# Optimization experiments

Hardware: AMD Instinct MI355X
Metric: run time of the kernel (lower is better)

Reference implementation:

```python
import jax, jax.numpy as jnp
import numpy as np

# ---- MACE hyperparameters (match init_kwargs) ----
R_MAX = 5.0      # radial cutoff
P_CUT = 6        # polynomial cutoff exponent
NUM_BESSEL = 8
C = 32           # hidden channels
N_NODES = 50000
N_EDGES = 800000
N_SPECIES = 10
N_GRAPHS = 32
AVG_NEIGH = 16.0
RADIAL_HIDDEN = 64
N_LM = 9                      # (lmax+1)^2, lmax=2
L_OF_LM = np.array([0, 1, 1, 1, 2, 2, 2, 2, 2])


def _sph_harm_l2(v):
    """Real spherical harmonics up to l=2, e3nn 'component' normalization.
    v: [E,3] unit vectors -> [E,9]."""
    x, y, z = v[:, 0], v[:, 1], v[:, 2]
    s3, s5, s15 = 3.0 ** 0.5, 5.0 ** 0.5, 15.0 ** 0.5
    return jnp.stack([
        jnp.ones_like(x),                 # l=0
        s3 * x, s3 * y, s3 * z,           # l=1
        s15 * x * y, s15 * y * z,         # l=2
        (s5 / 2.0) * (3.0 * z * z - 1.0),
        s15 * x * z,
        (s15 / 2.0) * (x * x - y * y),
    ], axis=-1)


def _radial_basis(r):
    """Bessel basis * polynomial cutoff. r: [E] -> [E, NUM_BESSEL]."""
    n = jnp.arange(1, NUM_BESSEL + 1, dtype=r.dtype)
    safe_r = jnp.maximum(r, 1e-9)
    bessel = jnp.sqrt(2.0 / R_MAX) * jnp.sin(n * jnp.pi * safe_r[:, None] / R_MAX) / safe_r[:, None]
    u = r / R_MAX
    p = float(P_CUT)
    fcut = (1.0 - ((p + 1.0) * (p + 2.0) / 2.0) * u ** P_CUT
            + p * (p + 2.0) * u ** (P_CUT + 1)
            - (p * (p + 1.0) / 2.0) * u ** (P_CUT + 2))
    fcut = jnp.where(u < 1.0, fcut, 0.0)
    return bessel * fcut[:, None]


def setup_inputs() -> dict:
    key = jax.random.key(0)
    ks = jax.random.split(key, 12)
    positions = 1.5 * jax.random.normal(ks[0], (N_NODES, 3), dtype=jnp.float32)
    shifts = jnp.zeros((N_EDGES, 3), dtype=jnp.float32)
    species = jax.random.randint(ks[1], (N_NODES,), 0, N_SPECIES)
    node_attrs = jax.nn.one_hot(species, N_SPECIES, dtype=jnp.float32)
    edge_index = jax.random.randint(ks[2], (2, N_EDGES), 0, N_NODES)
    batch = jnp.sort(jax.random.randint(ks[3], (N_NODES,), 0, N_GRAPHS))
    # learned parameters
    W_embed = jax.random.normal(ks[4], (N_SPECIES, C), jnp.float32) / np.sqrt(N_SPECIES)
    rW1 = jax.random.normal(ks[5], (NUM_BESSEL, RADIAL_HIDDEN), jnp.float32) / np.sqrt(NUM_BESSEL)
    rb1 = jnp.zeros((RADIAL_HIDDEN,), jnp.float32)
    rW2 = jax.random.normal(ks[6], (RADIAL_HIDDEN, RADIAL_HIDDEN), jnp.float32) / np.sqrt(RADIAL_HIDDEN)
    rb2 = jnp.zeros((RADIAL_HIDDEN,), jnp.float32)
    rW3 = jax.random.normal(ks[7], (RADIAL_HIDDEN, C * 3), jnp.float32) / np.sqrt(RADIAL_HIDDEN)
    W_mix = jax.random.normal(ks[8], (3, C, C), jnp.float32) / np.sqrt(C)   # per-l channel mixing
    w_quad = jax.random.normal(ks[9], (3,), jnp.float32) * 0.1              # correlation-2 invariant weights
    W_readout = jax.random.normal(ks[10], (C,), jnp.float32) / np.sqrt(C)
    atomic_energies = jax.random.normal(ks[11], (N_SPECIES,), jnp.float32)
    return {"node_attrs": node_attrs, "positions": positions, "shifts": shifts,
            "W_embed": W_embed, "rW1": rW1, "rb1": rb1, "rW2": rW2, "rb2": rb2,
            "rW3": rW3, "W_mix": W_mix, "w_quad": w_quad, "W_readout": W_readout,
            "atomic_energies": atomic_energies, "edge_index": edge_index, "batch": batch}


def reference(node_attrs, positions, shifts, W_embed, rW1, rb1, rW2, rb2, rW3,
              W_mix, w_quad, W_readout, atomic_energies, edge_index, batch):
    sender, receiver = edge_index[0], edge_index[1]
    # edge vectors / lengths (get_edge_vectors_and_lengths)
    vec = positions[receiver] - positions[sender] + shifts          # [E,3]
    length = jnp.linalg.norm(vec, axis=-1)                          # [E]
    unit = vec / jnp.maximum(length, 1e-9)[:, None]
    # radial embedding (Bessel * polynomial cutoff) -> MLP -> per-(channel,l) weights
    rb = _radial_basis(length)                                      # [E,8]
    h1 = jax.nn.silu(rb @ rW1 + rb1)
    h2 = jax.nn.silu(h1 @ rW2 + rb2)
    R = (h2 @ rW3).reshape(-1, C, 3)                                # [E,C,3]
    Y = _sph_harm_l2(unit)                                          # [E,9]
    # node embedding (LinearNodeEmbeddingBlock)
    h = node_attrs @ W_embed                                        # [N,C]
    # channelwise CG tensor product message (scalar source x Y_l -> l) + scatter-sum
    l_of_lm = jnp.asarray(L_OF_LM)
    msg = R[:, :, l_of_lm] * h[sender][:, :, None] * Y[:, None, :]  # [E,C,9]
    A = jax.ops.segment_sum(msg, receiver, num_segments=N_NODES) / AVG_NEIGH  # [N,C,9]
    # per-l linear channel mixing (o3.Linear)
    W_lm = W_mix[l_of_lm]                                           # [9,C,C]
    A2 = jnp.einsum('mcd,ncm->ndm', W_lm, A)                        # [N,C,9]
    # symmetric contraction (correlation 2): rotation-invariant features
    sq = A2 * A2                                                    # [N,C,9]
    onehot_l = jax.nn.one_hot(l_of_lm, 3, dtype=A2.dtype)           # [9,3]
    l_norms = jnp.einsum('ncm,ml->ncl', sq, onehot_l)               # [N,C,3]
    B = A2[:, :, 0] + l_norms @ w_quad                              # [N,C]
    # readout + atomic reference energies, pooled per graph
    node_e = B @ W_readout + node_attrs @ atomic_energies           # [N]
    graph_e = jax.ops.segment_sum(node_e, batch, num_segments=N_GRAPHS)
    return graph_e
```

## Files before the change

### kernel.cpp

```cpp
#include <hip/hip_runtime.h>
#include <hip/hip_bf16.h>

#define NNODES 50000
#define NEDGES 800000
#define NGRAPHS 32
#define NSPEC 10
#define CC 32
#define RH 64
#define NB 8

#define EBLK 128
#define NCHUNK (NEDGES / EBLK)
#define GSTR 136
#define YSTRF 132
#define ASTR 72
#define RBSTR 40
#define SCAN_N 53248

typedef __bf16 bf16x8 __attribute__((ext_vector_type(8)));
typedef float f32x4 __attribute__((ext_vector_type(4)));

__device__ __forceinline__ unsigned pack2bf(float a, float b) {
    return (unsigned)__bfloat16_as_ushort(__float2bfloat16(a)) |
           ((unsigned)__bfloat16_as_ushort(__float2bfloat16(b)) << 16);
}
__device__ __forceinline__ float silu(float x) { return x / (1.f + __expf(-x)); }

__global__ __launch_bounds__(256) void prep_hist_kernel(
    const float* __restrict__ attrs, const int* __restrict__ eidx,
    const float* __restrict__ rW1, const float* __restrict__ rb1,
    const float* __restrict__ rW2, const float* __restrict__ rW3,
    int* __restrict__ counts, int* __restrict__ rank, int* __restrict__ species,
    __hip_bfloat16* __restrict__ W1T, __hip_bfloat16* __restrict__ W2T,
    __hip_bfloat16* __restrict__ W3T) {
    __shared__ float at[256 * NSPEC];
    const int tid = threadIdx.x;
    int g = blockIdx.x * 256 + tid;
    if (g < NEDGES) rank[g] = atomicAdd(&counts[eidx[NEDGES + g]], 1);
    const int nbase = blockIdx.x * 256;
    if (nbase < NNODES) {
        for (int i = tid; i < 256 * NSPEC; i += 256) {
            int idx = nbase * NSPEC + i;
            at[i] = (idx < NNODES * NSPEC) ? attrs[idx] : 0.f;
        }
        __syncthreads();
        if (g < NNODES) {
            float acc = 0.f;
#pragma unroll
            for (int s = 0; s < NSPEC; ++s) acc += at[tid * NSPEC + s] * (float)s;
            species[g] = (int)(acc + 0.5f);
        }
    }
    if (g < 64 * 32) {
        int c = g >> 5, k = g & 31;
        float v = (k < 8) ? rW1[k * 64 + c] : ((k == 8) ? rb1[c] : 0.f);
        W1T[g] = __float2bfloat16(v);
    }
    if (g < 64 * 64) {
        int c = g >> 6, k = g & 63;
        W2T[g] = __float2bfloat16(rW2[k * 64 + c]);
    }
    if (g < 96 * 64) {
        int c = g >> 6, k = g & 63;
        W3T[g] = __float2bfloat16(rW3[k * 96 + c]);
    }
}

__global__ __launch_bounds__(1024) void scan_kernel(const int* __restrict__ counts,
                                                    int* __restrict__ offsets) {
    __shared__ int sums[1024];
    const int t = threadIdx.x;
    const int base = t * 52;
    int loc[52];
    int s = 0;
#pragma unroll
    for (int i = 0; i < 13; ++i) {
        int4 v = *(const int4*)&counts[base + i * 4];
        loc[i * 4 + 0] = v.x; loc[i * 4 + 1] = v.y;
        loc[i * 4 + 2] = v.z; loc[i * 4 + 3] = v.w;
        s += v.x + v.y + v.z + v.w;
    }
    sums[t] = s;
    __syncthreads();
    for (int off = 1; off < 1024; off <<= 1) {
        int add = (t >= off) ? sums[t - off] : 0;
        __syncthreads();
        sums[t] += add;
        __syncthreads();
    }
    int run = sums[t] - s;
#pragma unroll
    for (int i = 0; i < 13; ++i) {
        int4 o;
        o.x = run; run += loc[i * 4 + 0];
        o.y = run; run += loc[i * 4 + 1];
        o.z = run; run += loc[i * 4 + 2];
        o.w = run; run += loc[i * 4 + 3];
        *(int4*)&offsets[base + i * 4] = o;
    }
}

__global__ __launch_bounds__(256) void scatter_kernel(const int* __restrict__ eidx,
                                                      const int* __restrict__ offsets,
                                                      const int* __restrict__ rank,
                                                      int* __restrict__ perm) {
    int e = blockIdx.x * 256 + threadIdx.x;
    if (e >= NEDGES) return;
    int rcv = eidx[NEDGES + e];
    perm[offsets[rcv] + rank[e]] = e;
}

__global__ __launch_bounds__(576) void zero_bounds_kernel(const int* __restrict__ perm,
                                                          const int* __restrict__ eidx,
                                                          float* __restrict__ A) {
    const int c = blockIdx.x;
    const int t = threadIdx.x;
    const int slot = (t < 288) ? c * EBLK : (c * EBLK + EBLK - 1);
    const int e = perm[slot];
    const int rcv = eidx[NEDGES + e];
    A[(size_t)rcv * (CC * 9) + (t % 288)] = 0.f;
}

__device__ __forceinline__ void flushseg(float* __restrict__ A, int node, int cur,
                                         int nseg, int cbase, int j, bool wr8,
                                         float aj, float a8) {
    float* Ap = A + (size_t)node * (CC * 9) + cbase * 9;
    if (cur == 0 || cur == nseg - 1) {
        atomicAdd(Ap + j, aj);
        if (wr8) atomicAdd(Ap + 8, a8);
    } else {
        Ap[j] = aj;
        if (wr8) Ap[8] = a8;
    }
}

template <int P>
__device__ __forceinline__ void pass_store_reduce(
    const f32x4 (&acc3)[4][6], const int (&sp_r)[4][4],
    __hip_bfloat16* Gt, const float* Yt, const float* WembLds,
    const unsigned short* rcv_s, const unsigned long long* bal_s,
    float* __restrict__ A, int tid, int w, int lnlo, int q4) {
#pragma unroll
    for (int nti = 0; nti < 3; ++nti) {
        const int nt = P * 3 + nti;
        const int col = nt * 16 + lnlo;
        const int cch = col / 3;
        const int s = nti * 16 + lnlo;
#pragma unroll
        for (int mt = 0; mt < 4; ++mt) {
            const float f0 = acc3[mt][nt][0] * WembLds[sp_r[mt][0] * 32 + cch];
            const float f1 = acc3[mt][nt][1] * WembLds[sp_r[mt][1] * 32 + cch];
            const float f2 = acc3[mt][nt][2] * WembLds[sp_r[mt][2] * 32 + cch];
            const float f3 = acc3[mt][nt][3] * WembLds[sp_r[mt][3] * 32 + cch];
            uint2 pk;
            pk.x = pack2bf(f0, f1);
            pk.y = pack2bf(f2, f3);
            *(uint2*)&Gt[s * GSTR + w * 64 + mt * 16 + q4 * 4] = pk;
        }
    }
    __syncthreads();

    {
        const int c = tid >> 3;
        const int j = tid & 7;
        const bool m8 = (j == 7);
        const int l_j = (j == 0) ? 0 : ((j < 4) ? 1 : 2);
        const uint4* gj = (const uint4*)(Gt + (3 * c + l_j) * GSTR);
        const float4* yj = (const float4*)(Yt + j * YSTRF);
        const float4* y8f = (const float4*)(Yt + 8 * YSTRF);
        const unsigned long long b0 = bal_s[0], b1 = bal_s[1];
        const int nseg = __popcll(b0) + __popcll(b1);
        const int cbase = P * 16 + c;

        float aj = 0.f, a8 = 0.f;
        int cur = 0;
        int node = rcv_s[0];

        for (int ch = 0; ch < 16; ++ch) {
            unsigned msk = (unsigned)(((ch < 8) ? (b0 >> (ch * 8)) : (b1 >> ((ch - 8) * 8))) & 0xffull);
            if (ch == 0) msk &= ~1u;
            const uint4 gv = gj[ch];
            const float4 ya = yj[2 * ch];
            const float4 yb = yj[2 * ch + 1];
            float4 y8a = {0.f, 0.f, 0.f, 0.f}, y8b = {0.f, 0.f, 0.f, 0.f};
            if (m8) { y8a = y8f[2 * ch]; y8b = y8f[2 * ch + 1]; }
            const unsigned gw[4] = {gv.x, gv.y, gv.z, gv.w};
            const float yf[8] = {ya.x, ya.y, ya.z, ya.w, yb.x, yb.y, yb.z, yb.w};
            const float yf8[8] = {y8a.x, y8a.y, y8a.z, y8a.w, y8b.x, y8b.y, y8b.z, y8b.w};
#pragma unroll
            for (int i = 0; i < 8; ++i) {
                if (msk & (1u << i)) {
                    flushseg(A, node, cur, nseg, cbase, j, m8, aj, a8);
                    aj = 0.f; a8 = 0.f; ++cur;
                    node = rcv_s[ch * 8 + i];
                }
                const unsigned gu = gw[i >> 1];
                const float gf = __uint_as_float((i & 1) ? (gu & 0xffff0000u) : (gu << 16));
                aj = fmaf(gf, yf[i], aj);
                if (m8) a8 = fmaf(gf, yf8[i], a8);
            }
        }
        flushseg(A, node, cur, nseg, cbase, j, m8, aj, a8);
    }
    __syncthreads();
}

__global__ __launch_bounds__(EBLK, 3) void edge_kernel(
    const float* __restrict__ pos, const float* __restrict__ shifts,
    const int* __restrict__ eidx, const int* __restrict__ perm,
    const __hip_bfloat16* __restrict__ W1T, const __hip_bfloat16* __restrict__ W2T,
    const __hip_bfloat16* __restrict__ W3T, const float* __restrict__ rb2,
    const int* __restrict__ species, const float* __restrict__ Wemb,
    float* __restrict__ A) {
    __shared__ __align__(16) short smem_u[128 * ASTR];
    __shared__ __align__(16) float Yt[9 * YSTRF];
    __shared__ float WembLds[NSPEC * CC];
    __shared__ float rb2L[RH];
    __shared__ unsigned short rcv_s[EBLK];
    __shared__ unsigned char spec_s[EBLK];
    __shared__ unsigned long long bal_s[2];

    __hip_bfloat16* act = (__hip_bfloat16*)smem_u;
    __hip_bfloat16* Gt = (__hip_bfloat16*)smem_u;
    __hip_bfloat16* rbA = (__hip_bfloat16*)smem_u;

    const int tid = threadIdx.x;
    const int lane = tid & 63;
    const int w = tid >> 6;
    const int lnlo = lane & 15;
    const int q4 = lane >> 4;

    const int slot = blockIdx.x * EBLK + tid;
    const int eid = perm[slot];
    const int snd = eidx[eid];
    const int rcv = eidx[NEDGES + eid];

    const float vx = pos[rcv * 3 + 0] - pos[snd * 3 + 0] + shifts[eid * 3 + 0];
    const float vy = pos[rcv * 3 + 1] - pos[snd * 3 + 1] + shifts[eid * 3 + 1];
    const float vz = pos[rcv * 3 + 2] - pos[snd * 3 + 2] + shifts[eid * 3 + 2];
    const float r = sqrtf(vx * vx + vy * vy + vz * vz);
    const float safe_r = fmaxf(r, 1e-9f);
    const float rinv = 1.f / safe_r;
    const float ux = vx * rinv, uy = vy * rinv, uz = vz * rinv;

    {
        const float s3 = 1.7320508075688772f;
        const float s15 = 3.872983346207417f;
        const float s15h = 1.9364916731037085f;
        const float s5h = 1.118033988749895f;
        Yt[0 * YSTRF + tid] = 1.f;
        Yt[1 * YSTRF + tid] = s3 * ux;
        Yt[2 * YSTRF + tid] = s3 * uy;
        Yt[3 * YSTRF + tid] = s3 * uz;
        Yt[4 * YSTRF + tid] = s15 * ux * uy;
        Yt[5 * YSTRF + tid] = s15 * uy * uz;
        Yt[6 * YSTRF + tid] = s5h * (3.f * uz * uz - 1.f);
        Yt[7 * YSTRF + tid] = s15 * ux * uz;
        Yt[8 * YSTRF + tid] = s15h * (ux * ux - uy * uy);
        rcv_s[tid] = (unsigned short)rcv;
        spec_s[tid] = (unsigned char)species[snd];
        for (int i = tid; i < NSPEC * CC; i += EBLK) WembLds[i] = Wemb[i];
        if (tid < RH) rb2L[tid] = rb2[tid];
    }

    {
        const float u = r * 0.2f;
        const float u2 = u * u;
        const float u6 = u2 * u2 * u2;
        const float u7 = u6 * u;
        const float u8v = u7 * u;
        float fcut = 1.f - 28.f * u6 + 48.f * u7 - 21.f * u8v;
        fcut = (u < 1.f) ? fcut : 0.f;
        const float pref = 0.632455532f * rinv * fcut;
        float rb[NB];
#pragma unroll
        for (int k = 0; k < NB; ++k) {
            const float fk = (float)(k + 1) * 0.628318530718f;
            rb[k] = __sinf(fk * safe_r) * pref;
        }
        uint4 v0, v1;
        v0.x = pack2bf(rb[0], rb[1]); v0.y = pack2bf(rb[2], rb[3]);
        v0.z = pack2bf(rb[4], rb[5]); v0.w = pack2bf(rb[6], rb[7]);
        v1.x = 0x3F80u; v1.y = 0u; v1.z = 0u; v1.w = 0u;
        uint4 vz4 = {0u, 0u, 0u, 0u};
        *(uint4*)&rbA[tid * RBSTR + 0] = v0;
        *(uint4*)&rbA[tid * RBSTR + 8] = v1;
        *(uint4*)&rbA[tid * RBSTR + 16] = vz4;
        *(uint4*)&rbA[tid * RBSTR + 24] = vz4;
    }

    __syncthreads();
    {
        const bool head = (tid == 0) || (rcv_s[tid] != rcv_s[tid - 1]);
        const unsigned long long bal = __ballot(head);
        if ((tid & 63) == 0) bal_s[tid >> 6] = bal;
    }

    f32x4 acc1[4][4];
#pragma unroll
    for (int jt = 0; jt < 4; ++jt)
#pragma unroll
        for (int et = 0; et < 4; ++et) acc1[jt][et] = (f32x4){0.f, 0.f, 0.f, 0.f};
    {
        bf16x8 wf[4], af[4];
#pragma unroll
        for (int jt = 0; jt < 4; ++jt)
            wf[jt] = *(const bf16x8*)&W1T[(jt * 16 + lnlo) * 32 + q4 * 8];
#pragma unroll
        for (int et = 0; et < 4; ++et)
            af[et] = *(const bf16x8*)&rbA[(w * 64 + et * 16 + lnlo) * RBSTR + q4 * 8];
        __syncthreads();
#pragma unroll
        for (int jt = 0; jt < 4; ++jt)
#pragma unroll
            for (int et = 0; et < 4; ++et)
                acc1[jt][et] = __builtin_amdgcn_mfma_f32_16x16x32_bf16(
                    wf[jt], af[et], acc1[jt][et], 0, 0, 0);
    }

#pragma unroll
    for (int jt = 0; jt < 4; ++jt) {
        const int ch0 = jt * 16 + q4 * 4;
#pragma unroll
        for (int et = 0; et < 4; ++et) {
            const int e = w * 64 + et * 16 + lnlo;
            uint2 pk;
            pk.x = pack2bf(silu(acc1[jt][et][0]), silu(acc1[jt][et][1]));
            pk.y = pack2bf(silu(acc1[jt][et][2]), silu(acc1[jt][et][3]));
            *(uint2*)&act[e * ASTR + ch0] = pk;
        }
    }
    __syncthreads();

    f32x4 acc2[4][4];
#pragma unroll
    for (int jt = 0; jt < 4; ++jt)
#pragma unroll
        for (int et = 0; et < 4; ++et) acc2[jt][et] = (f32x4){0.f, 0.f, 0.f, 0.f};
    {
        bf16x8 wf[4][2], af[4][2];
#pragma unroll
        for (int jt = 0; jt < 4; ++jt)
#pragma unroll
            for (int kk = 0; kk < 2; ++kk)
                wf[jt][kk] = *(const bf16x8*)&W2T[(jt * 16 + lnlo) * 64 + kk * 32 + q4 * 8];
#pragma unroll
        for (int et = 0; et < 4; ++et)
#pragma unroll
            for (int kk = 0; kk < 2; ++kk)
                af[et][kk] = *(const bf16x8*)&act[(w * 64 + et * 16 + lnlo) * ASTR + kk * 32 + q4 * 8];
#pragma unroll
        for (int kk = 0; kk < 2; ++kk)
#pragma unroll
            for (int jt = 0; jt < 4; ++jt)
#pragma unroll
                for (int et = 0; et < 4; ++et)
                    acc2[jt][et] = __builtin_amdgcn_mfma_f32_16x16x32_bf16(
                        wf[jt][kk], af[et][kk], acc2[jt][et], 0, 0, 0);
    }
    __syncthreads();

#pragma unroll
    for (int jt = 0; jt < 4; ++jt) {
        const int ch0 = jt * 16 + q4 * 4;
        const float4 bv = *(const float4*)&rb2L[ch0];
#pragma unroll
        for (int et = 0; et < 4; ++et) {
            const int e = w * 64 + et * 16 + lnlo;
            uint2 pk;
            pk.x = pack2bf(silu(acc2[jt][et][0] + bv.x), silu(acc2[jt][et][1] + bv.y));
            pk.y = pack2bf(silu(acc2[jt][et][2] + bv.z), silu(acc2[jt][et][3] + bv.w));
            *(uint2*)&act[e * ASTR + ch0] = pk;
        }
    }
    __syncthreads();

    f32x4 acc3[4][6];
#pragma unroll
    for (int mt = 0; mt < 4; ++mt)
#pragma unroll
        for (int nt = 0; nt < 6; ++nt) acc3[mt][nt] = (f32x4){0.f, 0.f, 0.f, 0.f};
    {
        bf16x8 a3[4][2], b3[6][2];
#pragma unroll
        for (int mt = 0; mt < 4; ++mt)
#pragma unroll
            for (int kk = 0; kk < 2; ++kk)
                a3[mt][kk] = *(const bf16x8*)&act[(w * 64 + mt * 16 + lnlo) * ASTR + kk * 32 + q4 * 8];
#pragma unroll
        for (int nt = 0; nt < 6; ++nt)
#pragma unroll
            for (int kk = 0; kk < 2; ++kk)
                b3[nt][kk] = *(const bf16x8*)&W3T[(nt * 16 + lnlo) * 64 + kk * 32 + q4 * 8];
#pragma unroll
        for (int kk = 0; kk < 2; ++kk)
#pragma unroll
            for (int mt = 0; mt < 4; ++mt)
#pragma unroll
                for (int nt = 0; nt < 6; ++nt)
                    acc3[mt][nt] = __builtin_amdgcn_mfma_f32_16x16x32_bf16(
                        a3[mt][kk], b3[nt][kk], acc3[mt][nt], 0, 0, 0);
    }
    __syncthreads();

    int sp_r[4][4];
#pragma unroll
    for (int mt = 0; mt < 4; ++mt)
#pragma unroll
        for (int rr = 0; rr < 4; ++rr)
            sp_r[mt][rr] = (int)spec_s[w * 64 + mt * 16 + q4 * 4 + rr];

    pass_store_reduce<0>(acc3, sp_r, Gt, Yt, WembLds, rcv_s, bal_s, A, tid, w, lnlo, q4);
    pass_store_reduce<1>(acc3, sp_r, Gt, Yt, WembLds, rcv_s, bal_s, A, tid, w, lnlo, q4);
}

__global__ __launch_bounds__(256) void node_kernel(
    const float* __restrict__ A, const float* __restrict__ Wmix,
    const float* __restrict__ wquad, const float* __restrict__ Wread,
    const float* __restrict__ attrs, const float* __restrict__ ae,
    const int* __restrict__ batch, const int* __restrict__ counts,
    float* __restrict__ out) {
    __shared__ float Ald[8][CC * 9];
    __shared__ float ne_s[8];
    __shared__ int g_s[8];
    const int t = threadIdx.x;
    const int ln = t >> 5;
    const int d = t & 31;
    const int n = blockIdx.x * 8 + ln;

    const float sc = (counts[n] != 0) ? (1.f / 16.f) : 0.f;
    const float* Arow = A + (size_t)n * (CC * 9);
#pragma unroll
    for (int i = 0; i < 9; ++i) Ald[ln][d + 32 * i] = Arow[d + 32 * i] * sc;
    __syncthreads();

    float A2[9];
#pragma unroll
    for (int m = 0; m < 9; ++m) {
        const int l = (m == 0) ? 0 : ((m < 4) ? 1 : 2);
        float acc = 0.f;
#pragma unroll
        for (int cch = 0; cch < CC; ++cch)
            acc = fmaf(Wmix[(l * CC + cch) * CC + d], Ald[ln][cch * 9 + m], acc);
        A2[m] = acc;
    }

    const float q0 = wquad[0], q1 = wquad[1], q2 = wquad[2];
    const float n0 = A2[0] * A2[0];
    const float n1 = A2[1] * A2[1] + A2[2] * A2[2] + A2[3] * A2[3];
    const float n2 = A2[4] * A2[4] + A2[5] * A2[5] + A2[6] * A2[6] + A2[7] * A2[7] + A2[8] * A2[8];
    const float B = A2[0] + n0 * q0 + n1 * q1 + n2 * q2;

    float v = B * Wread[d];
#pragma unroll
    for (int off = 16; off; off >>= 1) v += __shfl_xor(v, off, 32);

    if (d == 0) {
        float ne = v;
#pragma unroll
        for (int s = 0; s < NSPEC; ++s) ne += attrs[n * NSPEC + s] * ae[s];
        ne_s[ln] = ne;
        g_s[ln] = batch[n];
    }
    __syncthreads();
    if (t == 0) {
        float acc = ne_s[0];
        int g = g_s[0];
#pragma unroll
        for (int i = 1; i < 8; ++i) {
            if (g_s[i] == g) acc += ne_s[i];
            else { atomicAdd(&out[g], acc); g = g_s[i]; acc = ne_s[i]; }
        }
        atomicAdd(&out[g], acc);
    }
}

extern "C" void kernel_launch(void* const* d_in, const int* in_sizes, int n_in,
                              void* d_out, int out_size, void* d_ws, size_t ws_size,
                              hipStream_t stream) {
    const float* attrs  = (const float*)d_in[0];
    const float* pos    = (const float*)d_in[1];
    const float* shifts = (const float*)d_in[2];
    const float* Wemb   = (const float*)d_in[3];
    const float* rW1    = (const float*)d_in[4];
    const float* rb1    = (const float*)d_in[5];
    const float* rW2    = (const float*)d_in[6];
    const float* rb2    = (const float*)d_in[7];
    const float* rW3    = (const float*)d_in[8];
    const float* Wmix   = (const float*)d_in[9];
    const float* wquad  = (const float*)d_in[10];
    const float* Wread  = (const float*)d_in[11];
    const float* ae     = (const float*)d_in[12];
    const int* eidx     = (const int*)d_in[13];
    const int* batch    = (const int*)d_in[14];
    float* out = (float*)d_out;

    char* wsp = (char*)d_ws;
    float* A      = (float*)wsp;  wsp += (size_t)NNODES * CC * 9 * 4;
    int* rank     = (int*)A;
    int* perm     = (int*)wsp;    wsp += (size_t)NEDGES * 4;
    int* offsets  = (int*)wsp;    wsp += (size_t)SCAN_N * 4;
    int* counts   = (int*)wsp;    wsp += (size_t)SCAN_N * 4;
    int* species  = (int*)wsp;    wsp += (size_t)NNODES * 4;
    __hip_bfloat16* W1T = (__hip_bfloat16*)wsp; wsp += 64 * 32 * 2;
    __hip_bfloat16* W2T = (__hip_bfloat16*)wsp; wsp += 64 * 64 * 2;
    __hip_bfloat16* W3T = (__hip_bfloat16*)wsp; wsp += 96 * 64 * 2;

    hipMemsetAsync(counts, 0, (size_t)SCAN_N * sizeof(int), stream);
    hipMemsetAsync(out, 0, NGRAPHS * sizeof(float), stream);

    prep_hist_kernel<<<NEDGES / 256, 256, 0, stream>>>(attrs, eidx, rW1, rb1, rW2, rW3,
                                                       counts, rank, species, W1T, W2T, W3T);
    scan_kernel<<<1, 1024, 0, stream>>>(counts, offsets);
    scatter_kernel<<<NEDGES / 256, 256, 0, stream>>>(eidx, offsets, rank, perm);
    zero_bounds_kernel<<<NCHUNK, 576, 0, stream>>>(perm, eidx, A);

    edge_kernel<<<NCHUNK, EBLK, 0, stream>>>(pos, shifts, eidx, perm,
                                             W1T, W2T, W3T, rb2, species, Wemb, A);
    node_kernel<<<NNODES / 8, 256, 0, stream>>>(A, Wmix, wquad, Wread, attrs, ae, batch,
                                                counts, out);
}
```

Measured before the change: 309.5 us.

## Prefetch segment-scan operands, split accumulators, use sine recurrence, drop memset

In the edge kernel's segmented reduction, the next chunk's G and Y values are loaded one iteration ahead, and a branch-free fast path handles chunks with no segment boundary. Two independent accumulators shorten the FMA dependency chain. The eight Bessel sines now come from one sincos plus a Chebyshev recurrence instead of eight sin calls, and the output zeroing moves into the scan kernel so one memset launch goes away. The recurrence can accumulate small rounding error, and the prefetch reads one chunk past the end, which is why the Yt array gets padding.

```diff
diff --git a/kernel.cpp b/kernel.cpp
--- a/kernel.cpp
+++ b/kernel.cpp
@@ -67,9 +67,11 @@
 }
 
 __global__ __launch_bounds__(1024) void scan_kernel(const int* __restrict__ counts,
-                                                    int* __restrict__ offsets) {
+                                                    int* __restrict__ offsets,
+                                                    float* __restrict__ out) {
     __shared__ int sums[1024];
     const int t = threadIdx.x;
+    if (t < NGRAPHS) out[t] = 0.f;
     const int base = t * 52;
     int loc[52];
     int s = 0;
@@ -172,35 +174,62 @@
         const int nseg = __popcll(b0) + __popcll(b1);
         const int cbase = P * 16 + c;
 
-        float aj = 0.f, a8 = 0.f;
+        float aj0 = 0.f, aj1 = 0.f, a80 = 0.f, a81 = 0.f;
         int cur = 0;
         int node = rcv_s[0];
 
+        uint4 gv = gj[0];
+        float4 ya = yj[0], yb = yj[1];
+        float4 y8a = {0, 0, 0, 0}, y8b = {0, 0, 0, 0};
+        if (m8) { y8a = y8f[0]; y8b = y8f[1]; }
+
         for (int ch = 0; ch < 16; ++ch) {
+            uint4 gv_n = gj[ch + 1];
+            float4 ya_n = yj[2 * ch + 2], yb_n = yj[2 * ch + 3];
+            float4 y8a_n = y8a, y8b_n = y8b;
+            if (m8) { y8a_n = y8f[2 * ch + 2]; y8b_n = y8f[2 * ch + 3]; }
+
             unsigned msk = (unsigned)(((ch < 8) ? (b0 >> (ch * 8)) : (b1 >> ((ch - 8) * 8))) & 0xffull);
             if (ch == 0) msk &= ~1u;
-            const uint4 gv = gj[ch];
-            const float4 ya = yj[2 * ch];
-            const float4 yb = yj[2 * ch + 1];
-            float4 y8a = {0.f, 0.f, 0.f, 0.f}, y8b = {0.f, 0.f, 0.f, 0.f};
-            if (m8) { y8a = y8f[2 * ch]; y8b = y8f[2 * ch + 1]; }
             const unsigned gw[4] = {gv.x, gv.y, gv.z, gv.w};
             const float yf[8] = {ya.x, ya.y, ya.z, ya.w, yb.x, yb.y, yb.z, yb.w};
             const float yf8[8] = {y8a.x, y8a.y, y8a.z, y8a.w, y8b.x, y8b.y, y8b.z, y8b.w};
-#pragma unroll
-            for (int i = 0; i < 8; ++i) {
-                if (msk & (1u << i)) {
-                    flushseg(A, node, cur, nseg, cbase, j, m8, aj, a8);
-                    aj = 0.f; a8 = 0.f; ++cur;
-                    node = rcv_s[ch * 8 + i];
+
+            if (msk == 0) {
+#pragma unroll
+                for (int i = 0; i < 8; i += 2) {
+                    const unsigned gu = gw[i >> 1];
+                    const float gf0 = __uint_as_float(gu << 16);
+                    const float gf1 = __uint_as_float(gu & 0xffff0000u);
+                    aj0 = fmaf(gf0, yf[i], aj0);
+                    aj1 = fmaf(gf1, yf[i + 1], aj1);
+                    if (m8) {
+                        a80 = fmaf(gf0, yf8[i], a80);
+                        a81 = fmaf(gf1, yf8[i + 1], a81);
+                    }
                 }
-                const unsigned gu = gw[i >> 1];
-                const float gf = __uint_as_float((i & 1) ? (gu & 0xffff0000u) : (gu << 16));
-                aj = fmaf(gf, yf[i], aj);
-                if (m8) a8 = fmaf(gf, yf8[i], a8);
+            } else {
+#pragma unroll
+                for (int i = 0; i < 8; ++i) {
+                    if (msk & (1u << i)) {
+                        flushseg(A, node, cur, nseg, cbase, j, m8, aj0 + aj1, a80 + a81);
+                        aj0 = aj1 = a80 = a81 = 0.f;
+                        ++cur;
+                        node = rcv_s[ch * 8 + i];
+                    }
+                    const unsigned gu = gw[i >> 1];
+                    const float gf = __uint_as_float((i & 1) ? (gu & 0xffff0000u) : (gu << 16));
+                    if (i & 1) aj1 = fmaf(gf, yf[i], aj1);
+                    else       aj0 = fmaf(gf, yf[i], aj0);
+                    if (m8) {
+                        if (i & 1) a81 = fmaf(gf, yf8[i], a81);
+                        else       a80 = fmaf(gf, yf8[i], a80);
+                    }
+                }
             }
-        }
-        flushseg(A, node, cur, nseg, cbase, j, m8, aj, a8);
+            gv = gv_n; ya = ya_n; yb = yb_n; y8a = y8a_n; y8b = y8b_n;
+        }
+        flushseg(A, node, cur, nseg, cbase, j, m8, aj0 + aj1, a80 + a81);
     }
     __syncthreads();
 }
@@ -213,7 +242,7 @@
     const int* __restrict__ species, const float* __restrict__ Wemb,
     float* __restrict__ A) {
     __shared__ __align__(16) short smem_u[128 * ASTR];
-    __shared__ __align__(16) float Yt[9 * YSTRF];
+    __shared__ __align__(16) float Yt[9 * YSTRF + 4];
     __shared__ float WembLds[NSPEC * CC];
     __shared__ float rb2L[RH];
     __shared__ unsigned short rcv_s[EBLK];
@@ -272,11 +301,18 @@
         float fcut = 1.f - 28.f * u6 + 48.f * u7 - 21.f * u8v;
         fcut = (u < 1.f) ? fcut : 0.f;
         const float pref = 0.632455532f * rinv * fcut;
+        const float x = 0.628318530718f * safe_r;
+        float s1, c1;
+        __sincosf(x, &s1, &c1);
+        const float tc = 2.f * c1;
         float rb[NB];
-#pragma unroll
-        for (int k = 0; k < NB; ++k) {
-            const float fk = (float)(k + 1) * 0.628318530718f;
-            rb[k] = __sinf(fk * safe_r) * pref;
+        float sp = 0.f, sc = s1;
+        rb[0] = sc * pref;
+#pragma unroll
+        for (int k = 1; k < NB; ++k) {
+            const float sn = tc * sc - sp;
+            sp = sc; sc = sn;
+            rb[k] = sc * pref;
         }
         uint4 v0, v1;
         v0.x = pack2bf(rb[0], rb[1]); v0.y = pack2bf(rb[2], rb[3]);
@@ -507,11 +543,10 @@
     __hip_bfloat16* W3T = (__hip_bfloat16*)wsp; wsp += 96 * 64 * 2;
 
     hipMemsetAsync(counts, 0, (size_t)SCAN_N * sizeof(int), stream);
-    hipMemsetAsync(out, 0, NGRAPHS * sizeof(float), stream);
 
     prep_hist_kernel<<<NEDGES / 256, 256, 0, stream>>>(attrs, eidx, rW1, rb1, rW2, rW3,
                                                        counts, rank, species, W1T, W2T, W3T);
-    scan_kernel<<<1, 1024, 0, stream>>>(counts, offsets);
+    scan_kernel<<<1, 1024, 0, stream>>>(counts, offsets, out);
     scatter_kernel<<<NEDGES / 256, 256, 0, stream>>>(eidx, offsets, rank, perm);
     zero_bounds_kernel<<<NCHUNK, 576, 0, stream>>>(perm, eidx, A);
 
```

Result: no change. 315.5 us (+1.9%).

## Store spherical harmonics as bf16, use sine recurrence, fold output memset into scan

Applied to the files above, without the earlier changes.

The per-edge spherical harmonics table in LDS is now bf16 rather than fp32, which halves its shared-memory footprint and the reads in the scatter-reduce loop, at some cost in precision. The eight Bessel sines now come from one sincos plus a Chebyshev-style recurrence instead of eight separate sine calls. The output zeroing moves from a separate hipMemsetAsync into the scan kernel, removing one launch. These ideas are independent of each other, and the recurrence and bf16 storage add small numerical error.

```diff
diff --git a/kernel.cpp b/kernel.cpp
--- a/kernel.cpp
+++ b/kernel.cpp
@@ -12,7 +12,7 @@
 #define EBLK 128
 #define NCHUNK (NEDGES / EBLK)
 #define GSTR 136
-#define YSTRF 132
+#define YSTR 136
 #define ASTR 72
 #define RBSTR 40
 #define SCAN_N 53248
@@ -67,9 +67,11 @@
 }
 
 __global__ __launch_bounds__(1024) void scan_kernel(const int* __restrict__ counts,
-                                                    int* __restrict__ offsets) {
+                                                    int* __restrict__ offsets,
+                                                    float* __restrict__ out) {
     __shared__ int sums[1024];
     const int t = threadIdx.x;
+    if (t < NGRAPHS) out[t] = 0.f;
     const int base = t * 52;
     int loc[52];
     int s = 0;
@@ -137,7 +139,7 @@
 template <int P>
 __device__ __forceinline__ void pass_store_reduce(
     const f32x4 (&acc3)[4][6], const int (&sp_r)[4][4],
-    __hip_bfloat16* Gt, const float* Yt, const float* WembLds,
+    __hip_bfloat16* Gt, const __hip_bfloat16* Yt, const float* WembLds,
     const unsigned short* rcv_s, const unsigned long long* bal_s,
     float* __restrict__ A, int tid, int w, int lnlo, int q4) {
 #pragma unroll
@@ -166,8 +168,8 @@
         const bool m8 = (j == 7);
         const int l_j = (j == 0) ? 0 : ((j < 4) ? 1 : 2);
         const uint4* gj = (const uint4*)(Gt + (3 * c + l_j) * GSTR);
-        const float4* yj = (const float4*)(Yt + j * YSTRF);
-        const float4* y8f = (const float4*)(Yt + 8 * YSTRF);
+        const uint4* yj = (const uint4*)(Yt + j * YSTR);
+        const uint4* y8p = (const uint4*)(Yt + 8 * YSTR);
         const unsigned long long b0 = bal_s[0], b1 = bal_s[1];
         const int nseg = __popcll(b0) + __popcll(b1);
         const int cbase = P * 16 + c;
@@ -180,13 +182,12 @@
             unsigned msk = (unsigned)(((ch < 8) ? (b0 >> (ch * 8)) : (b1 >> ((ch - 8) * 8))) & 0xffull);
             if (ch == 0) msk &= ~1u;
             const uint4 gv = gj[ch];
-            const float4 ya = yj[2 * ch];
-            const float4 yb = yj[2 * ch + 1];
-            float4 y8a = {0.f, 0.f, 0.f, 0.f}, y8b = {0.f, 0.f, 0.f, 0.f};
-            if (m8) { y8a = y8f[2 * ch]; y8b = y8f[2 * ch + 1]; }
+            const uint4 yv = yj[ch];
+            uint4 yv8 = {0, 0, 0, 0};
+            if (m8) yv8 = y8p[ch];
             const unsigned gw[4] = {gv.x, gv.y, gv.z, gv.w};
-            const float yf[8] = {ya.x, ya.y, ya.z, ya.w, yb.x, yb.y, yb.z, yb.w};
-            const float yf8[8] = {y8a.x, y8a.y, y8a.z, y8a.w, y8b.x, y8b.y, y8b.z, y8b.w};
+            const unsigned yw[4] = {yv.x, yv.y, yv.z, yv.w};
+            const unsigned yw8[4] = {yv8.x, yv8.y, yv8.z, yv8.w};
 #pragma unroll
             for (int i = 0; i < 8; ++i) {
                 if (msk & (1u << i)) {
@@ -194,10 +195,15 @@
                     aj = 0.f; a8 = 0.f; ++cur;
                     node = rcv_s[ch * 8 + i];
                 }
-                const unsigned gu = gw[i >> 1];
+                const unsigned gu = gw[i >> 1], yu = yw[i >> 1];
                 const float gf = __uint_as_float((i & 1) ? (gu & 0xffff0000u) : (gu << 16));
-                aj = fmaf(gf, yf[i], aj);
-                if (m8) a8 = fmaf(gf, yf8[i], a8);
+                const float yf = __uint_as_float((i & 1) ? (yu & 0xffff0000u) : (yu << 16));
+                aj = fmaf(gf, yf, aj);
+                if (m8) {
+                    const unsigned zu = yw8[i >> 1];
+                    const float zf = __uint_as_float((i & 1) ? (zu & 0xffff0000u) : (zu << 16));
+                    a8 = fmaf(gf, zf, a8);
+                }
             }
         }
         flushseg(A, node, cur, nseg, cbase, j, m8, aj, a8);
@@ -213,7 +219,7 @@
     const int* __restrict__ species, const float* __restrict__ Wemb,
     float* __restrict__ A) {
     __shared__ __align__(16) short smem_u[128 * ASTR];
-    __shared__ __align__(16) float Yt[9 * YSTRF];
+    __shared__ __align__(16) __hip_bfloat16 Yt[9 * YSTR + 4];
     __shared__ float WembLds[NSPEC * CC];
     __shared__ float rb2L[RH];
     __shared__ unsigned short rcv_s[EBLK];
@@ -248,15 +254,15 @@
         const float s15 = 3.872983346207417f;
         const float s15h = 1.9364916731037085f;
         const float s5h = 1.118033988749895f;
-        Yt[0 * YSTRF + tid] = 1.f;
-        Yt[1 * YSTRF + tid] = s3 * ux;
-        Yt[2 * YSTRF + tid] = s3 * uy;
-        Yt[3 * YSTRF + tid] = s3 * uz;
-        Yt[4 * YSTRF + tid] = s15 * ux * uy;
-        Yt[5 * YSTRF + tid] = s15 * uy * uz;
-        Yt[6 * YSTRF + tid] = s5h * (3.f * uz * uz - 1.f);
-        Yt[7 * YSTRF + tid] = s15 * ux * uz;
-        Yt[8 * YSTRF + tid] = s15h * (ux * ux - uy * uy);
+        Yt[0 * YSTR + tid] = __float2bfloat16(1.f);
+        Yt[1 * YSTR + tid] = __float2bfloat16(s3 * ux);
+        Yt[2 * YSTR + tid] = __float2bfloat16(s3 * uy);
+        Yt[3 * YSTR + tid] = __float2bfloat16(s3 * uz);
+        Yt[4 * YSTR + tid] = __float2bfloat16(s15 * ux * uy);
+        Yt[5 * YSTR + tid] = __float2bfloat16(s15 * uy * uz);
+        Yt[6 * YSTR + tid] = __float2bfloat16(s5h * (3.f * uz * uz - 1.f));
+        Yt[7 * YSTR + tid] = __float2bfloat16(s15 * ux * uz);
+        Yt[8 * YSTR + tid] = __float2bfloat16(s15h * (ux * ux - uy * uy));
         rcv_s[tid] = (unsigned short)rcv;
         spec_s[tid] = (unsigned char)species[snd];
         for (int i = tid; i < NSPEC * CC; i += EBLK) WembLds[i] = Wemb[i];
@@ -272,11 +278,18 @@
         float fcut = 1.f - 28.f * u6 + 48.f * u7 - 21.f * u8v;
         fcut = (u < 1.f) ? fcut : 0.f;
         const float pref = 0.632455532f * rinv * fcut;
+        const float x = 0.628318530718f * safe_r;
+        float s1, c1;
+        __sincosf(x, &s1, &c1);
+        const float tc = 2.f * c1;
         float rb[NB];
-#pragma unroll
-        for (int k = 0; k < NB; ++k) {
-            const float fk = (float)(k + 1) * 0.628318530718f;
-            rb[k] = __sinf(fk * safe_r) * pref;
+        float sp = 0.f, sc = s1;
+        rb[0] = sc * pref;
+#pragma unroll
+        for (int k = 1; k < NB; ++k) {
+            const float sn = tc * sc - sp;
+            sp = sc; sc = sn;
+            rb[k] = sc * pref;
         }
         uint4 v0, v1;
         v0.x = pack2bf(rb[0], rb[1]); v0.y = pack2bf(rb[2], rb[3]);
@@ -507,11 +520,10 @@
     __hip_bfloat16* W3T = (__hip_bfloat16*)wsp; wsp += 96 * 64 * 2;
 
     hipMemsetAsync(counts, 0, (size_t)SCAN_N * sizeof(int), stream);
-    hipMemsetAsync(out, 0, NGRAPHS * sizeof(float), stream);
 
     prep_hist_kernel<<<NEDGES / 256, 256, 0, stream>>>(attrs, eidx, rW1, rb1, rW2, rW3,
                                                        counts, rank, species, W1T, W2T, W3T);
-    scan_kernel<<<1, 1024, 0, stream>>>(counts, offsets);
+    scan_kernel<<<1, 1024, 0, stream>>>(counts, offsets, out);
     scatter_kernel<<<NEDGES / 256, 256, 0, stream>>>(eidx, offsets, rank, perm);
     zero_bounds_kernel<<<NCHUNK, 576, 0, stream>>>(perm, eidx, A);
 
```

Result: no change. 310.7 us (+0.4%).
